# Performance work log

Measured on AMD Instinct MI355X. Metric: run time of the kernel, lower is better.

## Reference

```python
import jax, jax.numpy as jnp
import numpy as np

GROUP_SIZE = 64
M, K, N, RANK = 4096, 4096, 4096, 32


def setup_inputs() -> dict:
    key = jax.random.key(0)
    ks = jax.random.split(key, 7)
    x = jax.random.normal(ks[0], (M, K), dtype=jnp.float32)
    # int4 weight residual in [-8, 7]
    q_w = jax.random.randint(ks[1], (K, N), -8, 8, dtype=jnp.int32)
    # positive per-group weight scales, shape (K // group_size, N)
    wscales = jax.random.uniform(ks[2], (K // GROUP_SIZE, N), dtype=jnp.float32) * 0.01 + 1e-4
    lora_down = jax.random.normal(ks[3], (K, RANK), dtype=jnp.float32) * 0.02
    lora_up = jax.random.normal(ks[4], (RANK, N), dtype=jnp.float32) * 0.02
    # smoothing factors, strictly positive
    smooth = jax.random.uniform(ks[5], (K,), dtype=jnp.float32) + 0.5
    bias = jax.random.normal(ks[6], (N,), dtype=jnp.float32)
    return {"x": x, "q_w": q_w, "wscales": wscales, "lora_down": lora_down,
            "lora_up": lora_up, "smooth": smooth, "bias": bias}


def reference(x, q_w, wscales, lora_down, lora_up, smooth, bias):
    G = GROUP_SIZE
    m, k = x.shape
    n = q_w.shape[1]
    ng = k // G  # groups along K

    # smooth activation: move outliers into weights
    x_smooth = x / smooth[None, :]

    # per-group symmetric int4 quantize + dequantize of activations
    xg = x_smooth.reshape(m, ng, G)
    ascales = jnp.maximum(jnp.max(jnp.abs(xg), axis=-1) / 7.0, 1e-8)  # (m, ng)
    qx = jnp.clip(jnp.round(xg / ascales[..., None]), -8.0, 7.0)
    x_dq = (qx * ascales[..., None]).reshape(m, k)

    # dequantize int4 weight residual: grouped along K
    W_dq = (q_w.astype(jnp.float32).reshape(ng, G, n) * wscales[:, None, :]).reshape(k, n)

    # simulated int4 GEMM + fp LoRA residual + bias
    y_main = x_dq @ W_dq
    y_lora = (x @ lora_down) @ lora_up
    return y_main + y_lora + bias[None, :]
```

## Files before the change

kernel.cpp:

```cpp
#include <hip/hip_runtime.h>
#include <hip/hip_bf16.h>
#include <stdint.h>

#define GSIZE 64
#define MDIM 4096
#define KDIM 4096
#define NDIM 4096
#define RANK 32
#define KE   4160
#define NG   64
#define NSPLIT 8

#define B_QUANT 4096
#define B_WPREP (B_QUANT + 65 * 64)
#define B_LORAT (B_WPREP + 32 * NSPLIT)

typedef __bf16 bf16x4 __attribute__((ext_vector_type(4)));
typedef __bf16 bf16x8 __attribute__((ext_vector_type(8)));
typedef float  f32x4  __attribute__((ext_vector_type(4)));

#define GPTR(p) ((__attribute__((address_space(1))) void*)(uintptr_t)(p))
#define LPTR(p) ((__attribute__((address_space(3))) void*)(p))

__global__ __launch_bounds__(256) void k_prep(const float* __restrict__ x,
                                              const int*   __restrict__ qw,
                                              const float* __restrict__ wsc,
                                              const float* __restrict__ ld,
                                              const float* __restrict__ lu,
                                              const float* __restrict__ smooth,
                                              __bf16* __restrict__ A,
                                              __bf16* __restrict__ Wt,
                                              float* __restrict__ tws) {
    __shared__ __attribute__((aligned(16))) char smem[10240];
    int b   = blockIdx.x;
    int tid = threadIdx.x;

    if (b < B_QUANT) {
        int row = b;
        const float4* xr4 = (const float4*)(x + (size_t)row * KDIM);
        const float4* sm4 = (const float4*)smooth;
        __bf16* ar = A + (size_t)row * KE;
        #pragma unroll
        for (int p = 0; p < 4; ++p) {
            int i4 = p * 256 + tid;
            float4 xv = xr4[i4];
            float4 sv = sm4[i4];
            float4 xs = {xv.x * __builtin_amdgcn_rcpf(sv.x),
                         xv.y * __builtin_amdgcn_rcpf(sv.y),
                         xv.z * __builtin_amdgcn_rcpf(sv.z),
                         xv.w * __builtin_amdgcn_rcpf(sv.w)};
            float a = fmaxf(fmaxf(fabsf(xs.x), fabsf(xs.y)),
                            fmaxf(fabsf(xs.z), fabsf(xs.w)));
            #pragma unroll
            for (int off = 1; off < 16; off <<= 1)
                a = fmaxf(a, __shfl_xor(a, off, 64));
            float ascale = fmaxf(a * (1.0f / 7.0f), 1e-8f);
            float rin = __builtin_amdgcn_rcpf(ascale);
            float q0 = fminf(fmaxf(rintf(xs.x * rin), -8.f), 7.f);
            float q1 = fminf(fmaxf(rintf(xs.y * rin), -8.f), 7.f);
            float q2 = fminf(fmaxf(rintf(xs.z * rin), -8.f), 7.f);
            float q3 = fminf(fmaxf(rintf(xs.w * rin), -8.f), 7.f);
            bf16x4 av = {(__bf16)(q0 * ascale), (__bf16)(q1 * ascale),
                         (__bf16)(q2 * ascale), (__bf16)(q3 * ascale)};
            *(bf16x4*)(ar + i4 * 4) = av;
        }
        return;
    }

    if (b < B_WPREP) {
        __bf16 (*tile)[68] = (__bf16(*)[68])smem;
        int idx = b - B_QUANT;
        int n0 = (idx & 63) * 64;
        int kt = idx >> 6;
        int k0 = kt * 64;
        int tr = tid >> 4;
        int tc = (tid & 15) * 4;
        if (kt < NG) {
            float4 ws = *(const float4*)(wsc + (size_t)kt * NDIM + n0 + tc);
            #pragma unroll
            for (int r = tr; r < 64; r += 16) {
                int4 q = *(const int4*)(qw + (size_t)(k0 + r) * NDIM + n0 + tc);
                tile[r][tc + 0] = (__bf16)((float)q.x * ws.x);
                tile[r][tc + 1] = (__bf16)((float)q.y * ws.y);
                tile[r][tc + 2] = (__bf16)((float)q.z * ws.z);
                tile[r][tc + 3] = (__bf16)((float)q.w * ws.w);
            }
        } else {
            #pragma unroll
            for (int r = tr; r < 64; r += 16) {
                if (r < RANK) {
                    float4 lv = *(const float4*)(lu + (size_t)r * NDIM + n0 + tc);
                    tile[r][tc + 0] = (__bf16)lv.x;
                    tile[r][tc + 1] = (__bf16)lv.y;
                    tile[r][tc + 2] = (__bf16)lv.z;
                    tile[r][tc + 3] = (__bf16)lv.w;
                } else {
                    tile[r][tc + 0] = (__bf16)0.f;
                    tile[r][tc + 1] = (__bf16)0.f;
                    tile[r][tc + 2] = (__bf16)0.f;
                    tile[r][tc + 3] = (__bf16)0.f;
                }
            }
        }
        __syncthreads();
        int nn = tid >> 3;
        int ks = (tid & 7) * 8;
        #pragma unroll
        for (int p = 0; p < 2; ++p) {
            int n = nn + p * 32;
            bf16x8 v;
            #pragma unroll
            for (int e = 0; e < 8; ++e) v[e] = tile[ks + e][n];
            *(bf16x8*)(Wt + (size_t)(n0 + n) * KE + k0 + ks) = v;
        }
        return;
    }

    {
        __bf16* AsL = (__bf16*)smem;
        __bf16* BsL = (__bf16*)(smem + 8192);
        int idx  = b - B_WPREP;
        int m0    = (idx & 31) * 128;
        int sp    = idx >> 5;
        int kbase = sp * 512;
        int lane = tid & 63;
        int wave = tid >> 6;
        int quad = lane >> 4;
        int mrow = lane & 15;

        f32x4 z = {0.f, 0.f, 0.f, 0.f};
        f32x4 acc[2][2];
        acc[0][0] = z; acc[0][1] = z; acc[1][0] = z; acc[1][1] = z;

        for (int step = 0; step < 16; ++step) {
            int kk = kbase + step * 32;
            #pragma unroll
            for (int it = 0; it < 2; ++it) {
                int slot = it * 256 + tid;
                int r = slot >> 2;
                int g = (slot & 3) ^ (r & 3);
                const float* src = x + (size_t)(m0 + r) * KDIM + kk + g * 8;
                float4 a0 = *(const float4*)src;
                float4 a1 = *(const float4*)(src + 4);
                bf16x8 v = {(__bf16)a0.x, (__bf16)a0.y, (__bf16)a0.z, (__bf16)a0.w,
                            (__bf16)a1.x, (__bf16)a1.y, (__bf16)a1.z, (__bf16)a1.w};
                *(bf16x8*)(AsL + slot * 8) = v;
            }
            #pragma unroll
            for (int i2 = 0; i2 < 4; ++i2) {
                int j = i2 * 256 + tid;
                int r = j >> 5, n = j & 31;
                BsL[n * 32 + r] = (__bf16)ld[(size_t)(kk + r) * RANK + n];
            }
            __syncthreads();
            bf16x8 av[2], bv[2];
            #pragma unroll
            for (int i = 0; i < 2; ++i) {
                int row  = wave * 32 + i * 16 + mrow;
                int slot = row * 4 + (quad ^ (row & 3));
                av[i] = *(const bf16x8*)(AsL + slot * 8);
            }
            #pragma unroll
            for (int j = 0; j < 2; ++j)
                bv[j] = *(const bf16x8*)(BsL + (j * 16 + mrow) * 32 + quad * 8);
            #pragma unroll
            for (int i = 0; i < 2; ++i)
                #pragma unroll
                for (int j = 0; j < 2; ++j)
                    acc[i][j] = __builtin_amdgcn_mfma_f32_16x16x32_bf16(av[i], bv[j], acc[i][j], 0, 0, 0);
            __syncthreads();
        }
        float* tout = tws + (size_t)sp * MDIM * RANK;
        #pragma unroll
        for (int i = 0; i < 2; ++i)
            #pragma unroll
            for (int j = 0; j < 2; ++j)
                #pragma unroll
                for (int r = 0; r < 4; ++r) {
                    int rowg = m0 + wave * 32 + i * 16 + quad * 4 + r;
                    int col  = j * 16 + mrow;
                    tout[(size_t)rowg * RANK + col] = acc[i][j][r];
                }
    }
}

__global__ __launch_bounds__(256) void k_fin(const float* __restrict__ tws,
                                             __bf16* __restrict__ A) {
    int idx = blockIdx.x * 256 + threadIdx.x;
    int m = idx >> 4, cq = idx & 15;
    int c = cq * 4;
    bf16x4 v = {(__bf16)0.f, (__bf16)0.f, (__bf16)0.f, (__bf16)0.f};
    if (c < RANK) {
        f32x4 s = {0.f, 0.f, 0.f, 0.f};
        #pragma unroll
        for (int sp = 0; sp < NSPLIT; ++sp) {
            f32x4 p = *(const f32x4*)(tws + ((size_t)sp * MDIM + m) * RANK + c);
            s.x += p.x; s.y += p.y; s.z += p.z; s.w += p.w;
        }
        v[0] = (__bf16)s.x; v[1] = (__bf16)s.y; v[2] = (__bf16)s.z; v[3] = (__bf16)s.w;
    }
    *(bf16x4*)(A + (size_t)m * KE + KDIM + c) = v;
}

__global__ __launch_bounds__(256) void k_gemm(const __bf16* __restrict__ A,
                                              const __bf16* __restrict__ Wt,
                                              const float*  __restrict__ bias,
                                              float* __restrict__ out) {
    __shared__ __attribute__((aligned(16))) __bf16 As[128 * 64];
    __shared__ __attribute__((aligned(16))) __bf16 Bs[128 * 64];
    int tid  = threadIdx.x;
    int lane = tid & 63;
    int wave = tid >> 6;
    int quad = lane >> 4;
    int mrow = lane & 15;
    int wm = wave >> 1, wn = wave & 1;
    int m0 = blockIdx.y * 128, n0 = blockIdx.x * 128;

    f32x4 z = {0.f, 0.f, 0.f, 0.f};
    f32x4 acc[4][4];
    #pragma unroll
    for (int i = 0; i < 4; ++i)
        #pragma unroll
        for (int j = 0; j < 4; ++j) acc[i][j] = z;

    const __bf16* Ab = A  + (size_t)m0 * KE;
    const __bf16* Bb = Wt + (size_t)n0 * KE;

    for (int kt = 0; kt < KE / 64; ++kt) {
        int k0 = kt * 64;
        #pragma unroll
        for (int it = 0; it < 4; ++it) {
            int c = it * 256 + tid;
            int r = c >> 3;
            int g = (c & 7) ^ (r & 7);
            int ldsoff = (it * 256 + wave * 64) * 16;
            __builtin_amdgcn_global_load_lds(GPTR(Ab + (size_t)r * KE + k0 + g * 8),
                                             LPTR((char*)As + ldsoff), 16, 0, 0);
            __builtin_amdgcn_global_load_lds(GPTR(Bb + (size_t)r * KE + k0 + g * 8),
                                             LPTR((char*)Bs + ldsoff), 16, 0, 0);
        }
        __syncthreads();
        #pragma unroll
        for (int s = 0; s < 2; ++s) {
            bf16x8 av[4], bv[4];
            #pragma unroll
            for (int i = 0; i < 4; ++i) {
                int row  = wm * 64 + i * 16 + mrow;
                int slot = row * 8 + ((s * 4 + quad) ^ (row & 7));
                av[i] = *(const bf16x8*)(As + slot * 8);
            }
            #pragma unroll
            for (int j = 0; j < 4; ++j) {
                int row  = wn * 64 + j * 16 + mrow;
                int slot = row * 8 + ((s * 4 + quad) ^ (row & 7));
                bv[j] = *(const bf16x8*)(Bs + slot * 8);
            }
            #pragma unroll
            for (int i = 0; i < 4; ++i)
                #pragma unroll
                for (int j = 0; j < 4; ++j)
                    acc[i][j] = __builtin_amdgcn_mfma_f32_16x16x32_bf16(av[i], bv[j], acc[i][j], 0, 0, 0);
        }
        __syncthreads();
    }

    #pragma unroll
    for (int j = 0; j < 4; ++j) {
        int col = n0 + wn * 64 + j * 16 + mrow;
        float bvs = bias[col];
        #pragma unroll
        for (int i = 0; i < 4; ++i) {
            int rbase = m0 + wm * 64 + i * 16 + quad * 4;
            #pragma unroll
            for (int r = 0; r < 4; ++r)
                out[(size_t)(rbase + r) * NDIM + col] = acc[i][j][r] + bvs;
        }
    }
}

extern "C" void kernel_launch(void* const* d_in, const int* in_sizes, int n_in,
                              void* d_out, int out_size, void* d_ws, size_t ws_size,
                              hipStream_t stream) {
    const float* x    = (const float*)d_in[0];
    const int*   qw   = (const int*)  d_in[1];
    const float* wsc  = (const float*)d_in[2];
    const float* ld   = (const float*)d_in[3];
    const float* lu   = (const float*)d_in[4];
    const float* sm   = (const float*)d_in[5];
    const float* bias = (const float*)d_in[6];
    float* out = (float*)d_out;

    char* ws = (char*)d_ws;
    __bf16* A   = (__bf16*)ws;
    __bf16* Wt  = (__bf16*)(ws + (size_t)MDIM * KE * 2);
    float*  tws = (float*) (ws + (size_t)MDIM * KE * 4);

    k_prep<<<B_LORAT, 256, 0, stream>>>(x, qw, wsc, ld, lu, sm, A, Wt, tws);
    k_fin<<<(MDIM * 16) / 256, 256, 0, stream>>>(tws, A);
    k_gemm<<<dim3(NDIM / 128, MDIM / 128), 256, 0, stream>>>(A, Wt, bias, out);
}
```

Measured before the change: 352.0 us.

## Fuse activation smoothing and int4 quantization into the LoRA-down pass

Removes the separate 4096 per-row quantization blocks and instead quantizes activations inside the LoRA-down GEMM blocks, which already read x. Each thread keeps the smoothed values for two 32-wide K steps in registers, reduces the 64-wide group max with lane shuffles, then writes the quantized bf16 groups to A. This avoids reading x from global memory a second time, at the cost of more register pressure and extra work in the LoRA blocks.

```diff
diff --git a/kernel.cpp b/kernel.cpp
--- a/kernel.cpp
+++ b/kernel.cpp
@@ -11,8 +11,7 @@
 #define NG   64
 #define NSPLIT 8
 
-#define B_QUANT 4096
-#define B_WPREP (B_QUANT + 65 * 64)
+#define B_WPREP (65 * 64)
 #define B_LORAT (B_WPREP + 32 * NSPLIT)
 
 typedef __bf16 bf16x4 __attribute__((ext_vector_type(4)));
@@ -35,43 +34,10 @@
     int b   = blockIdx.x;
     int tid = threadIdx.x;
 
-    if (b < B_QUANT) {
-        int row = b;
-        const float4* xr4 = (const float4*)(x + (size_t)row * KDIM);
-        const float4* sm4 = (const float4*)smooth;
-        __bf16* ar = A + (size_t)row * KE;
-        #pragma unroll
-        for (int p = 0; p < 4; ++p) {
-            int i4 = p * 256 + tid;
-            float4 xv = xr4[i4];
-            float4 sv = sm4[i4];
-            float4 xs = {xv.x * __builtin_amdgcn_rcpf(sv.x),
-                         xv.y * __builtin_amdgcn_rcpf(sv.y),
-                         xv.z * __builtin_amdgcn_rcpf(sv.z),
-                         xv.w * __builtin_amdgcn_rcpf(sv.w)};
-            float a = fmaxf(fmaxf(fabsf(xs.x), fabsf(xs.y)),
-                            fmaxf(fabsf(xs.z), fabsf(xs.w)));
-            #pragma unroll
-            for (int off = 1; off < 16; off <<= 1)
-                a = fmaxf(a, __shfl_xor(a, off, 64));
-            float ascale = fmaxf(a * (1.0f / 7.0f), 1e-8f);
-            float rin = __builtin_amdgcn_rcpf(ascale);
-            float q0 = fminf(fmaxf(rintf(xs.x * rin), -8.f), 7.f);
-            float q1 = fminf(fmaxf(rintf(xs.y * rin), -8.f), 7.f);
-            float q2 = fminf(fmaxf(rintf(xs.z * rin), -8.f), 7.f);
-            float q3 = fminf(fmaxf(rintf(xs.w * rin), -8.f), 7.f);
-            bf16x4 av = {(__bf16)(q0 * ascale), (__bf16)(q1 * ascale),
-                         (__bf16)(q2 * ascale), (__bf16)(q3 * ascale)};
-            *(bf16x4*)(ar + i4 * 4) = av;
-        }
-        return;
-    }
-
     if (b < B_WPREP) {
         __bf16 (*tile)[68] = (__bf16(*)[68])smem;
-        int idx = b - B_QUANT;
-        int n0 = (idx & 63) * 64;
-        int kt = idx >> 6;
+        int n0 = (b & 63) * 64;
+        int kt = b >> 6;
         int k0 = kt * 64;
         int tr = tid >> 4;
         int tc = (tid & 15) * 4;
@@ -119,7 +85,7 @@
     {
         __bf16* AsL = (__bf16*)smem;
         __bf16* BsL = (__bf16*)(smem + 8192);
-        int idx  = b - B_WPREP;
+        int idx   = b - B_WPREP;
         int m0    = (idx & 31) * 128;
         int sp    = idx >> 5;
         int kbase = sp * 512;
@@ -128,47 +94,98 @@
         int quad = lane >> 4;
         int mrow = lane & 15;
 
+        int rr[2], gg[2];
+        #pragma unroll
+        for (int it = 0; it < 2; ++it) {
+            int slot = it * 256 + tid;
+            rr[it] = slot >> 2;
+            gg[it] = (slot & 3) ^ (rr[it] & 3);
+        }
+
         f32x4 z = {0.f, 0.f, 0.f, 0.f};
         f32x4 acc[2][2];
         acc[0][0] = z; acc[0][1] = z; acc[1][0] = z; acc[1][1] = z;
 
-        for (int step = 0; step < 16; ++step) {
-            int kk = kbase + step * 32;
+        float he[2][8];
+        float ho[2][8];
+        float am[2];
+
+        for (int dstep = 0; dstep < 8; ++dstep) {
+            #pragma unroll
+            for (int s2 = 0; s2 < 2; ++s2) {
+                int kk = kbase + (dstep * 2 + s2) * 32;
+                #pragma unroll
+                for (int it = 0; it < 2; ++it) {
+                    int r = rr[it], g = gg[it];
+                    const float* src = x + (size_t)(m0 + r) * KDIM + kk + g * 8;
+                    float4 a0 = *(const float4*)src;
+                    float4 a1 = *(const float4*)(src + 4);
+                    const float* sms = smooth + kk + g * 8;
+                    float4 s0 = *(const float4*)sms;
+                    float4 s1 = *(const float4*)(sms + 4);
+                    bf16x8 v = {(__bf16)a0.x, (__bf16)a0.y, (__bf16)a0.z, (__bf16)a0.w,
+                                (__bf16)a1.x, (__bf16)a1.y, (__bf16)a1.z, (__bf16)a1.w};
+                    *(bf16x8*)(AsL + (it * 256 + tid) * 8) = v;
+                    float* h = s2 ? ho[it] : he[it];
+                    h[0] = a0.x * __builtin_amdgcn_rcpf(s0.x);
+                    h[1] = a0.y * __builtin_amdgcn_rcpf(s0.y);
+                    h[2] = a0.z * __builtin_amdgcn_rcpf(s0.z);
+                    h[3] = a0.w * __builtin_amdgcn_rcpf(s0.w);
+                    h[4] = a1.x * __builtin_amdgcn_rcpf(s1.x);
+                    h[5] = a1.y * __builtin_amdgcn_rcpf(s1.y);
+                    h[6] = a1.z * __builtin_amdgcn_rcpf(s1.z);
+                    h[7] = a1.w * __builtin_amdgcn_rcpf(s1.w);
+                    float a = fmaxf(fmaxf(fmaxf(fabsf(h[0]), fabsf(h[1])),
+                                          fmaxf(fabsf(h[2]), fabsf(h[3]))),
+                                    fmaxf(fmaxf(fabsf(h[4]), fabsf(h[5])),
+                                          fmaxf(fabsf(h[6]), fabsf(h[7]))));
+                    am[it] = s2 ? fmaxf(am[it], a) : a;
+                }
+                #pragma unroll
+                for (int i2 = 0; i2 < 4; ++i2) {
+                    int j = i2 * 256 + tid;
+                    int r = j >> 5, n = j & 31;
+                    BsL[n * 32 + r] = (__bf16)ld[(size_t)(kk + r) * RANK + n];
+                }
+                __syncthreads();
+                bf16x8 av[2], bv[2];
+                #pragma unroll
+                for (int i = 0; i < 2; ++i) {
+                    int row  = wave * 32 + i * 16 + mrow;
+                    int slot = row * 4 + (quad ^ (row & 3));
+                    av[i] = *(const bf16x8*)(AsL + slot * 8);
+                }
+                #pragma unroll
+                for (int j = 0; j < 2; ++j)
+                    bv[j] = *(const bf16x8*)(BsL + (j * 16 + mrow) * 32 + quad * 8);
+                #pragma unroll
+                for (int i = 0; i < 2; ++i)
+                    #pragma unroll
+                    for (int j = 0; j < 2; ++j)
+                        acc[i][j] = __builtin_amdgcn_mfma_f32_16x16x32_bf16(av[i], bv[j], acc[i][j], 0, 0, 0);
+                __syncthreads();
+            }
+            int kk0 = kbase + dstep * 64;
             #pragma unroll
             for (int it = 0; it < 2; ++it) {
-                int slot = it * 256 + tid;
-                int r = slot >> 2;
-                int g = (slot & 3) ^ (r & 3);
-                const float* src = x + (size_t)(m0 + r) * KDIM + kk + g * 8;
-                float4 a0 = *(const float4*)src;
-                float4 a1 = *(const float4*)(src + 4);
-                bf16x8 v = {(__bf16)a0.x, (__bf16)a0.y, (__bf16)a0.z, (__bf16)a0.w,
-                            (__bf16)a1.x, (__bf16)a1.y, (__bf16)a1.z, (__bf16)a1.w};
-                *(bf16x8*)(AsL + slot * 8) = v;
-            }
-            #pragma unroll
-            for (int i2 = 0; i2 < 4; ++i2) {
-                int j = i2 * 256 + tid;
-                int r = j >> 5, n = j & 31;
-                BsL[n * 32 + r] = (__bf16)ld[(size_t)(kk + r) * RANK + n];
-            }
-            __syncthreads();
-            bf16x8 av[2], bv[2];
-            #pragma unroll
-            for (int i = 0; i < 2; ++i) {
-                int row  = wave * 32 + i * 16 + mrow;
-                int slot = row * 4 + (quad ^ (row & 3));
-                av[i] = *(const bf16x8*)(AsL + slot * 8);
-            }
-            #pragma unroll
-            for (int j = 0; j < 2; ++j)
-                bv[j] = *(const bf16x8*)(BsL + (j * 16 + mrow) * 32 + quad * 8);
-            #pragma unroll
-            for (int i = 0; i < 2; ++i)
-                #pragma unroll
-                for (int j = 0; j < 2; ++j)
-                    acc[i][j] = __builtin_amdgcn_mfma_f32_16x16x32_bf16(av[i], bv[j], acc[i][j], 0, 0, 0);
-            __syncthreads();
+                float a = am[it];
+                a = fmaxf(a, __shfl_xor(a, 1, 64));
+                a = fmaxf(a, __shfl_xor(a, 2, 64));
+                float ascale = fmaxf(a * (1.0f / 7.0f), 1e-8f);
+                float rin = __builtin_amdgcn_rcpf(ascale);
+                bf16x8 qe, qo;
+                #pragma unroll
+                for (int j = 0; j < 8; ++j) {
+                    float q0 = fminf(fmaxf(rintf(he[it][j] * rin), -8.f), 7.f);
+                    float q1 = fminf(fmaxf(rintf(ho[it][j] * rin), -8.f), 7.f);
+                    qe[j] = (__bf16)(q0 * ascale);
+                    qo[j] = (__bf16)(q1 * ascale);
+                }
+                int r = rr[it], g = gg[it];
+                __bf16* arow = A + (size_t)(m0 + r) * KE;
+                *(bf16x8*)(arow + kk0 + g * 8)      = qe;
+                *(bf16x8*)(arow + kk0 + 32 + g * 8) = qo;
+            }
         }
         float* tout = tws + (size_t)sp * MDIM * RANK;
         #pragma unroll
```

New measurement: 364.4 us. 1.04x slower.
